# Kernel optimization log

Measured on AMD Instinct MI355X. Metric: run time of the kernel, lower is better.

Reference implementation:

```python
import jax, jax.numpy as jnp
import numpy as np

SPATIAL_SCALE = 0.25
N, C, H, W = 8, 256, 128, 128
P = 100000
IMG = 512.0  # image-space extent (H / spatial_scale)


def setup_inputs() -> dict:
    key = jax.random.key(0)
    k1, k2, k3, k4 = jax.random.split(key, 4)
    features = jax.random.normal(k1, (N, C, H, W), dtype=jnp.float32)
    batch_idx = jax.random.randint(k2, (P,), 0, N).astype(jnp.float32)
    xy = jax.random.uniform(k3, (P, 2), dtype=jnp.float32) * IMG
    rois = jnp.concatenate([batch_idx[:, None], xy], axis=1)  # [P,3]: (b, x, y)
    return {"features": features, "rois": rois}


def _interp(features, rois, spatial_scale):
    n, c, h, w = features.shape
    b = rois[:, 0].astype(jnp.int32)
    x = rois[:, 1] * spatial_scale
    y = rois[:, 2] * spatial_scale
    # RoIAlign-style bilinear interpolation with boundary handling
    valid = (y >= -1.0) & (y <= h) & (x >= -1.0) & (x <= w)
    y = jnp.maximum(y, 0.0)
    x = jnp.maximum(x, 0.0)
    y_low = jnp.floor(y).astype(jnp.int32)
    x_low = jnp.floor(x).astype(jnp.int32)
    y_at_edge = y_low >= h - 1
    x_at_edge = x_low >= w - 1
    y_low = jnp.minimum(y_low, h - 1)
    x_low = jnp.minimum(x_low, w - 1)
    y_high = jnp.where(y_at_edge, y_low, y_low + 1)
    x_high = jnp.where(x_at_edge, x_low, x_low + 1)
    y = jnp.where(y_at_edge, y_low.astype(y.dtype), y)
    x = jnp.where(x_at_edge, x_low.astype(x.dtype), x)
    ly = y - y_low
    lx = x - x_low
    hy = 1.0 - ly
    hx = 1.0 - lx
    w1 = (hy * hx)[:, None]  # [P,1]
    w2 = (hy * lx)[:, None]
    w3 = (ly * hx)[:, None]
    w4 = (ly * lx)[:, None]
    # fancy-index gather: [P, C] per corner
    v1 = features[b, :, y_low, x_low]
    v2 = features[b, :, y_low, x_high]
    v3 = features[b, :, y_high, x_low]
    v4 = features[b, :, y_high, x_high]
    out = w1 * v1 + w2 * v2 + w3 * v3 + w4 * v4  # [P, C]
    return jnp.where(valid[:, None], out, 0.0)


def reference(features, rois):
    return _interp(features, rois, SPATIAL_SCALE)
```

## Files before the change

kernel.cpp:

```cpp
#include <hip/hip_runtime.h>

#define SCALE   0.25f
#define NBATCH  8
#define CCH     256
#define HH      128
#define WW      128
#define NBUCK   (NBATCH * HH)
#define CG      32
#define NCG     (CCH / CG)
#define CAP     160


__global__ __launch_bounds__(1024) void k_bin(
    const float* __restrict__ rois, int* __restrict__ cnt,
    int4* __restrict__ slots, int P)
{
    __shared__ int lhist[NBUCK];
    __shared__ int lbase[NBUCK];
    const int t = threadIdx.x;
    lhist[t] = 0;
    __syncthreads();

    int p = blockIdx.x * 1024 + t;
    int mybk = -1, mypos = 0;
    int4 myrec = make_int4(0, 0, 0, 0);
    if (p < P) {
        float fb = rois[3 * p];
        float fx = rois[3 * p + 1] * SCALE;
        float fy = rois[3 * p + 2] * SCALE;
        int b = (int)fb;
        bool valid = (fy >= -1.0f) && (fy <= (float)HH) &&
                     (fx >= -1.0f) && (fx <= (float)WW);
        float y = fmaxf(fy, 0.0f);
        float x = fmaxf(fx, 0.0f);
        int ylo = (int)floorf(y);
        int xlo = (int)floorf(x);
        float yf = y, xf = x;
        int xhi;
        if (ylo >= HH - 1) { ylo = HH - 1; yf = (float)ylo; }
        if (xlo >= WW - 1) { xlo = WW - 1; xhi = WW - 1; xf = (float)xlo; }
        else               { xhi = xlo + 1; }
        float ly = yf - (float)ylo;
        float lx = xf - (float)xlo;
        unsigned pk = (unsigned)xlo | ((unsigned)xhi << 8) | (valid ? 0u : 0x80000000u);
        int bk = b * HH + ylo;
        mybk  = bk;
        mypos = atomicAdd(&lhist[bk], 1);
        myrec = make_int4(p, (int)pk, __float_as_int(lx), __float_as_int(ly));
    }
    __syncthreads();
    int h = lhist[t];
    lbase[t] = h ? atomicAdd(&cnt[t], h) : 0;
    __syncthreads();
    if (mybk >= 0) {
        int idx = lbase[mybk] + mypos;
        if (idx < CAP) slots[mybk * CAP + idx] = myrec;
    }
}

__global__ __launch_bounds__(512, 8) void k_main(
    const float* __restrict__ feat, const int4* __restrict__ slots,
    const int* __restrict__ cnt_arr, float* __restrict__ out)
{
    const int bk = blockIdx.x & (NBUCK - 1);
    const int cg = blockIdx.x >> 10;
    const int cnt = min(cnt_arr[bk], CAP);
    if (cnt == 0) return;
    const int b  = bk >> 7;
    const int yl = bk & 127;
    const int yh = min(yl + 1, HH - 1);

    __shared__ __align__(16) float lds[CG * 256];

    const int t    = threadIdx.x;
    const int wv   = t >> 6;
    const int lane = t & 63;

    const float* base = feat + (size_t)(b * CCH + cg * CG) * (HH * WW);
    {
        const int row = lane >> 5;
        const int y   = row ? yh : yl;
        const int ql  = lane & 31;
#pragma unroll
        for (int k = 0; k < 4; ++k) {
            const int c = k * 8 + wv;
            const int f = (c >> 1) & 7;
            const float* g = base + (size_t)c * (HH * WW) + y * WW + ((ql ^ f) << 2);
            __builtin_amdgcn_global_load_lds(
                (const __attribute__((address_space(1))) unsigned int*)g,
                (__attribute__((address_space(3))) unsigned int*)&lds[c * 256],
                16, 0, 0);
        }
    }
    __syncthreads();

    const int sub = lane >> 4;
    const int cp  = lane & 15;
    const int c0  = cp << 1;
    const int fc  = cp & 7;
    const float* ldc0 = &lds[c0 * 256];
    const int4* sb = slots + bk * CAP;

    for (int ii = wv * 4; ii < cnt; ii += 32) {
        int i = ii + sub;
        bool act = (i < cnt);
        int4 r = sb[act ? i : cnt - 1];
        unsigned pk = (unsigned)r.y;
        float lx = __int_as_float(r.z);
        float ly = __int_as_float(r.w);
        float s  = ((int)pk < 0) ? 0.0f : 1.0f;
        float hy = (1.0f - ly) * s;
        float lys = ly * s;
        float hx = 1.0f - lx;
        float w1 = hy * hx, w2 = hy * lx, w3 = lys * hx, w4 = lys * lx;
        int xlo = pk & 255;
        int xhi = (pk >> 8) & 255;
        int slo = (((xlo >> 2) ^ fc) << 2) | (xlo & 3);
        int shi = (((xhi >> 2) ^ fc) << 2) | (xhi & 3);

        float v1 = ldc0[slo],       v2 = ldc0[shi];
        float v3 = ldc0[128 + slo], v4 = ldc0[128 + shi];
        float o0 = w1 * v1 + w2 * v2 + w3 * v3 + w4 * v4;
        v1 = ldc0[256 + slo];       v2 = ldc0[256 + shi];
        v3 = ldc0[384 + slo];       v4 = ldc0[384 + shi];
        float o1 = w1 * v1 + w2 * v2 + w3 * v3 + w4 * v4;

        if (act)
            *(float2*)(out + (size_t)r.x * CCH + cg * CG + c0) = make_float2(o0, o1);
    }
}

extern "C" void kernel_launch(void* const* d_in, const int* in_sizes, int n_in,
                              void* d_out, int out_size, void* d_ws, size_t ws_size,
                              hipStream_t stream) {
    const float* feat = (const float*)d_in[0];
    const float* rois = (const float*)d_in[1];
    float* out = (float*)d_out;
    const int P = in_sizes[1] / 3;

    int*  cnt   = (int*)d_ws;
    int4* slots = (int4*)((char*)d_ws + NBUCK * sizeof(int));

    hipMemsetAsync(cnt, 0, NBUCK * sizeof(int), stream);
    const int bb = (P + 1023) / 1024;
    k_bin<<<bb, 1024, 0, stream>>>(rois, cnt, slots, P);
    k_main<<<NCG * NBUCK, 512, 0, stream>>>(feat, slots, cnt, out);
}
```

Before: 237.2 us.

## Group four adjacent row buckets per block to share staged feature rows

Each block now handles four consecutive y-row buckets and 16 channels instead of one bucket and 32 channels. It stages five feature rows in LDS, so adjacent buckets share the overlapping row and redundant global reads of each row drop from two to about 1.25. Points are indexed across the four buckets through prefix offsets. This adds per-point bucket-selection arithmetic, uses narrower 8-byte channel writes per row of output, and gives fewer blocks with more work each.

After: 263.4 us. 1.11x slower.

```diff
diff --git a/kernel.cpp b/kernel.cpp
--- a/kernel.cpp
+++ b/kernel.cpp
@@ -6,9 +6,13 @@
 #define HH      128
 #define WW      128
 #define NBUCK   (NBATCH * HH)
-#define CG      32
-#define NCG     (CCH / CG)
 #define CAP     160
+
+#define CG2     16
+#define NCG2    (CCH / CG2)
+#define QB      4
+#define ROWS    (QB + 1)
+#define NQG     (HH / QB)
 
 
 __global__ __launch_bounds__(1024) void k_bin(
@@ -62,49 +66,54 @@
     const float* __restrict__ feat, const int4* __restrict__ slots,
     const int* __restrict__ cnt_arr, float* __restrict__ out)
 {
-    const int bk = blockIdx.x & (NBUCK - 1);
-    const int cg = blockIdx.x >> 10;
-    const int cnt = min(cnt_arr[bk], CAP);
-    if (cnt == 0) return;
-    const int b  = bk >> 7;
-    const int yl = bk & 127;
-    const int yh = min(yl + 1, HH - 1);
+    const int bq = blockIdx.x & (NBATCH * NQG - 1);
+    const int cg = blockIdx.x >> 8;
+    const int b  = bq >> 5;
+    const int qg = bq & (NQG - 1);
+    const int y0 = qg * QB;
+    const int bk0 = b * HH + y0;
 
-    __shared__ __align__(16) float lds[CG * 256];
+    const int n0 = min(cnt_arr[bk0 + 0], CAP);
+    const int n1 = min(cnt_arr[bk0 + 1], CAP);
+    const int n2 = min(cnt_arr[bk0 + 2], CAP);
+    const int n3 = min(cnt_arr[bk0 + 3], CAP);
+    const int P1 = n0, P2 = P1 + n1, P3 = P2 + n2;
+    const int tot = P3 + n3;
+    if (tot == 0) return;
+
+    __shared__ __align__(16) float lds[ROWS * CG2 * WW];
 
     const int t    = threadIdx.x;
     const int wv   = t >> 6;
     const int lane = t & 63;
 
-    const float* base = feat + (size_t)(b * CCH + cg * CG) * (HH * WW);
+    const float* base = feat + (size_t)(b * CCH + cg * CG2) * (HH * WW);
     {
-        const int row = lane >> 5;
-        const int y   = row ? yh : yl;
-        const int ql  = lane & 31;
+        const int ch = 2 * wv + (lane >> 5);
+        const int ql = lane & 31;
+        const float* gch = base + (size_t)ch * (HH * WW) + (((ql ^ wv) & 31) << 2);
 #pragma unroll
-        for (int k = 0; k < 4; ++k) {
-            const int c = k * 8 + wv;
-            const int f = (c >> 1) & 7;
-            const float* g = base + (size_t)c * (HH * WW) + y * WW + ((ql ^ f) << 2);
+        for (int r = 0; r < ROWS; ++r) {
+            const int y = min(y0 + r, HH - 1);
             __builtin_amdgcn_global_load_lds(
-                (const __attribute__((address_space(1))) unsigned int*)g,
-                (__attribute__((address_space(3))) unsigned int*)&lds[c * 256],
+                (const __attribute__((address_space(1))) unsigned int*)(gch + y * WW),
+                (__attribute__((address_space(3))) unsigned int*)&lds[(r * CG2 + 2 * wv) * WW],
                 16, 0, 0);
         }
     }
     __syncthreads();
 
-    const int sub = lane >> 4;
-    const int cp  = lane & 15;
+    const int sub = lane >> 3;
+    const int cp  = lane & 7;
     const int c0  = cp << 1;
-    const int fc  = cp & 7;
-    const float* ldc0 = &lds[c0 * 256];
-    const int4* sb = slots + bk * CAP;
 
-    for (int ii = wv * 4; ii < cnt; ii += 32) {
-        int i = ii + sub;
-        bool act = (i < cnt);
-        int4 r = sb[act ? i : cnt - 1];
+    for (int ii = wv * 8; ii < tot; ii += 64) {
+        int j = ii + sub;
+        bool act = (j < tot);
+        int jc = act ? j : tot - 1;
+        int q   = (jc >= P1) + (jc >= P2) + (jc >= P3);
+        int Pq  = (q == 0) ? 0 : (q == 1) ? P1 : (q == 2) ? P2 : P3;
+        int4 r = slots[(bk0 + q) * CAP + (jc - Pq)];
         unsigned pk = (unsigned)r.y;
         float lx = __int_as_float(r.z);
         float ly = __int_as_float(r.w);
@@ -115,18 +124,19 @@
         float w1 = hy * hx, w2 = hy * lx, w3 = lys * hx, w4 = lys * lx;
         int xlo = pk & 255;
         int xhi = (pk >> 8) & 255;
-        int slo = (((xlo >> 2) ^ fc) << 2) | (xlo & 3);
-        int shi = (((xhi >> 2) ^ fc) << 2) | (xhi & 3);
+        int slo = ((((xlo >> 2) ^ cp) & 31) << 2) | (xlo & 3);
+        int shi = ((((xhi >> 2) ^ cp) & 31) << 2) | (xhi & 3);
 
-        float v1 = ldc0[slo],       v2 = ldc0[shi];
-        float v3 = ldc0[128 + slo], v4 = ldc0[128 + shi];
+        const float* ld0 = &lds[(q * CG2 + c0) * WW];
+        float v1 = ld0[slo],            v2 = ld0[shi];
+        float v3 = ld0[CG2 * WW + slo], v4 = ld0[CG2 * WW + shi];
         float o0 = w1 * v1 + w2 * v2 + w3 * v3 + w4 * v4;
-        v1 = ldc0[256 + slo];       v2 = ldc0[256 + shi];
-        v3 = ldc0[384 + slo];       v4 = ldc0[384 + shi];
+        v1 = ld0[WW + slo];             v2 = ld0[WW + shi];
+        v3 = ld0[CG2 * WW + WW + slo];  v4 = ld0[CG2 * WW + WW + shi];
         float o1 = w1 * v1 + w2 * v2 + w3 * v3 + w4 * v4;
 
         if (act)
-            *(float2*)(out + (size_t)r.x * CCH + cg * CG + c0) = make_float2(o0, o1);
+            *(float2*)(out + (size_t)r.x * CCH + cg * CG2 + c0) = make_float2(o0, o1);
     }
 }
 
@@ -144,5 +154,5 @@
     hipMemsetAsync(cnt, 0, NBUCK * sizeof(int), stream);
     const int bb = (P + 1023) / 1024;
     k_bin<<<bb, 1024, 0, stream>>>(rois, cnt, slots, P);
-    k_main<<<NCG * NBUCK, 512, 0, stream>>>(feat, slots, cnt, out);
+    k_main<<<NCG2 * NBATCH * NQG, 512, 0, stream>>>(feat, slots, cnt, out);
 }
```

## Transpose feature rows to channel-interleaved LDS layout with float4 gathers and 64-channel groups

Applied to the files above, without the earlier changes.

Doubles the channel group to 64 and the block to 1024 threads. Each block loads its two feature rows with ordinary float4 global loads, then transposes them in LDS so that four channels sit contiguously per x position, with a rotation swizzle to avoid bank conflicts. Each lane now gathers float4 corners and writes a float4 output, and the next ROI record is prefetched one iteration ahead. This replaces the asynchronous global-to-LDS load with a register-staged transpose and halves the number of blocks, which may reduce occupancy and overlap.

Result: no change. 235.1 us (-0.9%).

```diff
diff --git a/kernel.cpp b/kernel.cpp
--- a/kernel.cpp
+++ b/kernel.cpp
@@ -6,9 +6,10 @@
 #define HH      128
 #define WW      128
 #define NBUCK   (NBATCH * HH)
-#define CG      32
+#define CAP     160
+
+#define CG      64
 #define NCG     (CCH / CG)
-#define CAP     160
 
 
 __global__ __launch_bounds__(1024) void k_bin(
@@ -58,7 +59,7 @@
     }
 }
 
-__global__ __launch_bounds__(512, 8) void k_main(
+__global__ __launch_bounds__(1024, 8) void k_main(
     const float* __restrict__ feat, const int4* __restrict__ slots,
     const int* __restrict__ cnt_arr, float* __restrict__ out)
 {
@@ -70,63 +71,69 @@
     const int yl = bk & 127;
     const int yh = min(yl + 1, HH - 1);
 
-    __shared__ __align__(16) float lds[CG * 256];
+    __shared__ __align__(16) float lds[2 * 128 * 64];
+    float4* lds4 = (float4*)lds;
 
-    const int t    = threadIdx.x;
+    const int t = threadIdx.x;
+
+    {
+        const int xq  = t & 31;
+        const int cq  = (t >> 5) & 15;
+        const int row = t >> 9;
+        const int y   = row ? yh : yl;
+        const float* g = feat + ((size_t)(b * CCH + cg * CG + 4 * cq) * HH + y) * WW + 4 * xq;
+        float4 f0 = *(const float4*)(g);
+        float4 f1 = *(const float4*)(g + HH * WW);
+        float4 f2 = *(const float4*)(g + 2 * HH * WW);
+        float4 f3 = *(const float4*)(g + 3 * HH * WW);
+        const int slot = (cq + xq) & 15;
+        float4* d = &lds4[(size_t)row * 2048 + (4 * xq) * 16 + slot];
+        d[0]  = make_float4(f0.x, f1.x, f2.x, f3.x);
+        d[16] = make_float4(f0.y, f1.y, f2.y, f3.y);
+        d[32] = make_float4(f0.z, f1.z, f2.z, f3.z);
+        d[48] = make_float4(f0.w, f1.w, f2.w, f3.w);
+    }
+
     const int wv   = t >> 6;
     const int lane = t & 63;
+    const int sub  = lane >> 4;
+    const int cq   = lane & 15;
+    const int4* sb = slots + bk * CAP;
 
-    const float* base = feat + (size_t)(b * CCH + cg * CG) * (HH * WW);
-    {
-        const int row = lane >> 5;
-        const int y   = row ? yh : yl;
-        const int ql  = lane & 31;
-#pragma unroll
-        for (int k = 0; k < 4; ++k) {
-            const int c = k * 8 + wv;
-            const int f = (c >> 1) & 7;
-            const float* g = base + (size_t)c * (HH * WW) + y * WW + ((ql ^ f) << 2);
-            __builtin_amdgcn_global_load_lds(
-                (const __attribute__((address_space(1))) unsigned int*)g,
-                (__attribute__((address_space(3))) unsigned int*)&lds[c * 256],
-                16, 0, 0);
-        }
-    }
+    int  ii = wv * 4;
+    int4 rc = make_int4(0, 0, 0, 0);
+    if (ii < cnt) rc = sb[min(ii + sub, cnt - 1)];
     __syncthreads();
 
-    const int sub = lane >> 4;
-    const int cp  = lane & 15;
-    const int c0  = cp << 1;
-    const int fc  = cp & 7;
-    const float* ldc0 = &lds[c0 * 256];
-    const int4* sb = slots + bk * CAP;
+    for (; ii < cnt; ii += 64) {
+        int4 r = rc;
+        int jn = ii + 64;
+        if (jn < cnt) rc = sb[min(jn + sub, cnt - 1)];
 
-    for (int ii = wv * 4; ii < cnt; ii += 32) {
-        int i = ii + sub;
-        bool act = (i < cnt);
-        int4 r = sb[act ? i : cnt - 1];
+        bool act = (ii + sub < cnt);
         unsigned pk = (unsigned)r.y;
         float lx = __int_as_float(r.z);
         float ly = __int_as_float(r.w);
         float s  = ((int)pk < 0) ? 0.0f : 1.0f;
-        float hy = (1.0f - ly) * s;
+        float hy  = (1.0f - ly) * s;
         float lys = ly * s;
-        float hx = 1.0f - lx;
+        float hx  = 1.0f - lx;
         float w1 = hy * hx, w2 = hy * lx, w3 = lys * hx, w4 = lys * lx;
         int xlo = pk & 255;
         int xhi = (pk >> 8) & 255;
-        int slo = (((xlo >> 2) ^ fc) << 2) | (xlo & 3);
-        int shi = (((xhi >> 2) ^ fc) << 2) | (xhi & 3);
+        int alo = xlo * 16 + ((cq + (xlo >> 2)) & 15);
+        int ahi = xhi * 16 + ((cq + (xhi >> 2)) & 15);
 
-        float v1 = ldc0[slo],       v2 = ldc0[shi];
-        float v3 = ldc0[128 + slo], v4 = ldc0[128 + shi];
-        float o0 = w1 * v1 + w2 * v2 + w3 * v3 + w4 * v4;
-        v1 = ldc0[256 + slo];       v2 = ldc0[256 + shi];
-        v3 = ldc0[384 + slo];       v4 = ldc0[384 + shi];
-        float o1 = w1 * v1 + w2 * v2 + w3 * v3 + w4 * v4;
+        float4 v1 = lds4[alo],        v2 = lds4[ahi];
+        float4 v3 = lds4[2048 + alo], v4 = lds4[2048 + ahi];
+        float4 o;
+        o.x = w1 * v1.x + w2 * v2.x + w3 * v3.x + w4 * v4.x;
+        o.y = w1 * v1.y + w2 * v2.y + w3 * v3.y + w4 * v4.y;
+        o.z = w1 * v1.z + w2 * v2.z + w3 * v3.z + w4 * v4.z;
+        o.w = w1 * v1.w + w2 * v2.w + w3 * v3.w + w4 * v4.w;
 
         if (act)
-            *(float2*)(out + (size_t)r.x * CCH + cg * CG + c0) = make_float2(o0, o1);
+            *(float4*)(out + (size_t)r.x * CCH + cg * CG + 4 * cq) = o;
     }
 }
 
@@ -144,5 +151,5 @@
     hipMemsetAsync(cnt, 0, NBUCK * sizeof(int), stream);
     const int bb = (P + 1023) / 1024;
     k_bin<<<bb, 1024, 0, stream>>>(rois, cnt, slots, P);
-    k_main<<<NCG * NBUCK, 512, 0, stream>>>(feat, slots, cnt, out);
+    k_main<<<NCG * NBUCK, 1024, 0, stream>>>(feat, slots, cnt, out);
 }
```
